# Kernel tuning notes

Measured on AMD Instinct MI355X. Metric: run time of the kernel, lower is better.

The kernel has to match this reference:

```python
import jax, jax.numpy as jnp
import numpy as np

B, S, DIN, DOUT = 4, 2048, 4096, 4096
W_SCALE = 64.0   # makes round(weight*scale) produce non-trivial int8 values
X_SCALE = 16.0   # input_scale so x*scale truncates to non-zero int32 values


def setup_inputs() -> dict:
    key = jax.random.key(0)
    k1, k2, k3 = jax.random.split(key, 3)
    # kaiming_uniform fan_in: bound = sqrt(6/fan_in)
    bound = float(np.sqrt(6.0 / DIN))
    weight = jax.random.uniform(k1, (DOUT, DIN), jnp.float32, -bound, bound)
    x = jax.random.normal(k2, (B, S, DIN), jnp.float32)
    bias = jax.random.normal(k3, (DOUT,), jnp.float32) * 0.01
    weight_scale = jnp.full((DOUT,), W_SCALE, jnp.float32)
    input_scale = jnp.full((1,), X_SCALE, jnp.float32)
    return {"x": x, "weight": weight, "bias": bias,
            "weight_scale": weight_scale, "input_scale": input_scale}


def reference(x, weight, bias, weight_scale, input_scale):
    # x = x * input_scale (pre-scale path of forward)
    xs = x * input_scale
    # fake-quant weights: round to int8 with wraparound, like torch .to(int8)
    w_int = jnp.round(weight * weight_scale[:, None]).astype(jnp.int8)
    # x.to(torch.int32): truncation toward zero
    x_int = xs.astype(jnp.int32)
    # F.linear on the integer-valued tensors (computed in f32: values are exact ints)
    acc = jnp.einsum('bsd,od->bso', x_int.astype(jnp.float32),
                     w_int.astype(jnp.float32))
    acc = acc + bias  # bias added inside linear
    # dequant: divide by per-channel weight_scale and the scalar input_scale
    out = acc / (weight_scale * input_scale)
    return out
```

## Files before the change

### kernel.cpp

```cpp
#include <hip/hip_runtime.h>

#define GM 8192
#define GN 4096
#define GK 4096

#define BM 256
#define BN 256
#define BK 64
#define NTILE (GK / BK)
#define SLOT 32768

using int4v = __attribute__((ext_vector_type(4))) int;

__global__ __launch_bounds__(256) void quant_xw_k(
    const float4* __restrict__ x, unsigned int* __restrict__ xq,
    const float4* __restrict__ w, unsigned int* __restrict__ wq,
    const float* __restrict__ wscale, const float* __restrict__ iscale,
    int n4x, int n4tot) {
    const float xs = *iscale;
    const int stride = gridDim.x * blockDim.x;
    for (int i = blockIdx.x * blockDim.x + threadIdx.x; i < n4tot; i += stride) {
        if (i < n4x) {
            float4 v = x[i];
            int q0 = (int)(v.x * xs);
            int q1 = (int)(v.y * xs);
            int q2 = (int)(v.z * xs);
            int q3 = (int)(v.w * xs);
            xq[i] = (unsigned int)(q0 & 0xff)
                  | ((unsigned int)(q1 & 0xff) << 8)
                  | ((unsigned int)(q2 & 0xff) << 16)
                  | ((unsigned int)(q3 & 0xff) << 24);
        } else {
            int j = i - n4x;
            float s = wscale[j >> 10];
            float4 v = w[j];
            int q0 = (int)rintf(v.x * s);
            int q1 = (int)rintf(v.y * s);
            int q2 = (int)rintf(v.z * s);
            int q3 = (int)rintf(v.w * s);
            wq[j] = (unsigned int)(q0 & 0xff)
                  | ((unsigned int)(q1 & 0xff) << 8)
                  | ((unsigned int)(q2 & 0xff) << 16)
                  | ((unsigned int)(q3 & 0xff) << 24);
        }
    }
}

__global__ __launch_bounds__(512, 2) void qlinear_gemm_i8(
    const signed char* __restrict__ Aq,
    const signed char* __restrict__ Bq,
    const float* __restrict__ bias,
    const float* __restrict__ wscale,
    const float* __restrict__ iscale,
    float* __restrict__ C) {
    __shared__ signed char smem[2 * SLOT];

    const int tid  = threadIdx.x;
    const int wave = tid >> 6;
    const int lane = tid & 63;
    const int m0 = blockIdx.x * BM;
    const int n0 = blockIdx.y * BN;
    const int wm = (wave >> 2) * 128;
    const int wn = (wave & 3) * 64;

    int4v acc[8][4];
#pragma unroll
    for (int i = 0; i < 8; ++i)
#pragma unroll
        for (int j = 0; j < 4; ++j)
            acc[i][j] = int4v{0, 0, 0, 0};

    const int kc = ((tid & 3) ^ ((tid >> 3) & 3)) * 16;
    const signed char* gA  = Aq + (size_t)(m0 + (tid >> 2)) * GK + kc;
    const signed char* gA2 = gA + (size_t)128 * GK;
    const signed char* gB  = Bq + (size_t)(n0 + (tid >> 2)) * GK + kc;
    const signed char* gB2 = gB + (size_t)128 * GK;
    const int dst = tid * 16;

    const int pos = (((lane >> 4) ^ ((lane >> 1) & 3))) * 16;
    const int fAo = (wm + (lane & 15)) * 64 + pos;
    const int fBo = 16384 + (wn + (lane & 15)) * 64 + pos;

#define GLL16(g, l)                                                     \
    __builtin_amdgcn_global_load_lds(                                   \
        (__attribute__((address_space(1))) void*)(void*)(g),            \
        (__attribute__((address_space(3))) void*)(void*)(l), 16, 0, 0)

#define STAGE(kb, soff)                                                 \
    do {                                                                \
        GLL16(gA  + (kb), smem + (soff) + dst);                         \
        GLL16(gA2 + (kb), smem + (soff) + 8192 + dst);                  \
        GLL16(gB  + (kb), smem + (soff) + 16384 + dst);                 \
        GLL16(gB2 + (kb), smem + (soff) + 24576 + dst);                 \
    } while (0)

#define DSR(off) (*(const int4v*)(smem + (off)))
#define MFMA(A, B, Cc) __builtin_amdgcn_mfma_i32_16x16x64_i8(A, B, Cc, 0, 0, 0)

#define PH(q)                                                           \
    __builtin_amdgcn_s_barrier();                                       \
    asm volatile("s_waitcnt lgkmcnt(0)" ::: "memory");                  \
    __builtin_amdgcn_sched_barrier(0);                                  \
    __builtin_amdgcn_s_setprio(1);                                      \
    acc[2*(q)  ][0] = MFMA(pa0, bfr0, acc[2*(q)  ][0]);                 \
    acc[2*(q)+1][0] = MFMA(pa1, bfr0, acc[2*(q)+1][0]);                 \
    acc[2*(q)  ][1] = MFMA(pa0, bfr1, acc[2*(q)  ][1]);                 \
    acc[2*(q)+1][1] = MFMA(pa1, bfr1, acc[2*(q)+1][1]);                 \
    acc[2*(q)  ][2] = MFMA(pa0, bfr2, acc[2*(q)  ][2]);                 \
    acc[2*(q)+1][2] = MFMA(pa1, bfr2, acc[2*(q)+1][2]);                 \
    acc[2*(q)  ][3] = MFMA(pa0, bfr3, acc[2*(q)  ][3]);                 \
    acc[2*(q)+1][3] = MFMA(pa1, bfr3, acc[2*(q)+1][3]);                 \
    __builtin_amdgcn_s_setprio(0);                                      \
    __builtin_amdgcn_s_barrier();

#define HALF(SOFF, STAGE_CODE)                                          \
    do {                                                                \
        STAGE_CODE;                                                     \
        bfr0 = DSR((SOFF) + fBo);                                       \
        bfr1 = DSR((SOFF) + fBo + 1024);                                \
        bfr2 = DSR((SOFF) + fBo + 2048);                                \
        bfr3 = DSR((SOFF) + fBo + 3072);                                \
        pa0  = DSR((SOFF) + fAo);                                       \
        pa1  = DSR((SOFF) + fAo + 1024);                                \
        PH(0)                                                           \
        pa0 = DSR((SOFF) + fAo + 2048);                                 \
        pa1 = DSR((SOFF) + fAo + 3072);                                 \
        PH(1)                                                           \
        pa0 = DSR((SOFF) + fAo + 4096);                                 \
        pa1 = DSR((SOFF) + fAo + 5120);                                 \
        PH(2)                                                           \
        pa0 = DSR((SOFF) + fAo + 6144);                                 \
        pa1 = DSR((SOFF) + fAo + 7168);                                 \
        asm volatile("s_waitcnt vmcnt(0)" ::: "memory");                \
        PH(3)                                                           \
    } while (0)

    STAGE(0, 0);
    asm volatile("s_waitcnt vmcnt(0)" ::: "memory");
    __builtin_amdgcn_s_barrier();
    __builtin_amdgcn_sched_barrier(0);

    int4v bfr0, bfr1, bfr2, bfr3, pa0, pa1;
    int kA = BK;
    int kB = 2 * BK;
    for (int it = 0; it < NTILE / 2; ++it) {
        HALF(0,    { STAGE(kA, SLOT); kA += 2 * BK; });
        HALF(SLOT, { if (kB < GK) { STAGE(kB, 0); kB += 2 * BK; } });
    }

    const float isc = *iscale;
#pragma unroll
    for (int ni = 0; ni < 4; ++ni) {
        const int col = n0 + wn + ni * 16 + (lane & 15);
        const float bs_ = bias[col];
        const float inv = 1.0f / (wscale[col] * isc);
#pragma unroll
        for (int mi = 0; mi < 8; ++mi) {
            const int row0 = m0 + wm + mi * 16 + (lane >> 4) * 4;
#pragma unroll
            for (int r = 0; r < 4; ++r) {
                C[(size_t)(row0 + r) * GN + col] =
                    ((float)acc[mi][ni][r] + bs_) * inv;
            }
        }
    }
#undef HALF
#undef PH
#undef DSR
#undef MFMA
#undef STAGE
#undef GLL16
}

extern "C" void kernel_launch(void* const* d_in, const int* in_sizes, int n_in,
                              void* d_out, int out_size, void* d_ws, size_t ws_size,
                              hipStream_t stream) {
    const float* x      = (const float*)d_in[0];
    const float* w      = (const float*)d_in[1];
    const float* bias   = (const float*)d_in[2];
    const float* wscale = (const float*)d_in[3];
    const float* iscale = (const float*)d_in[4];
    float* out = (float*)d_out;

    signed char* xq = (signed char*)d_ws;
    signed char* wq = xq + (size_t)GM * GK;

    const int n4x = GM * GK / 4;
    const int n4w = GN * GK / 4;
    quant_xw_k<<<3072, 256, 0, stream>>>((const float4*)x, (unsigned int*)xq,
                                         (const float4*)w, (unsigned int*)wq,
                                         wscale, iscale, n4x, n4x + n4w);

    dim3 grid(GM / BM, GN / BN);
    qlinear_gemm_i8<<<grid, 512, 0, stream>>>(xq, wq, bias, wscale, iscale, out);
}
```

Before: 411.7 us.

## Load B fragments directly to registers and triple-buffer A tiles in LDS

The weight (B) operand is no longer staged through shared memory. Each wave loads its B fragments straight from global memory into registers, double-buffered across iterations. The A tiles move to a three-slot LDS ring with a deeper prefetch distance, and each iteration has a single barrier instead of eight. This removes LDS traffic and barriers for B at the cost of uncoalesced-ish global reads for B (each wave reads its own rows, duplicated across the two M-waves) and higher register pressure.

```diff
diff --git a/kernel.cpp b/kernel.cpp
--- a/kernel.cpp
+++ b/kernel.cpp
@@ -8,7 +8,7 @@
 #define BN 256
 #define BK 64
 #define NTILE (GK / BK)
-#define SLOT 32768
+#define ASLOT 16384
 
 using int4v = __attribute__((ext_vector_type(4))) int;
 
@@ -53,7 +53,7 @@
     const float* __restrict__ wscale,
     const float* __restrict__ iscale,
     float* __restrict__ C) {
-    __shared__ signed char smem[2 * SLOT];
+    __shared__ signed char smem[3 * ASLOT];
 
     const int tid  = threadIdx.x;
     const int wave = tid >> 6;
@@ -73,79 +73,115 @@
     const int kc = ((tid & 3) ^ ((tid >> 3) & 3)) * 16;
     const signed char* gA  = Aq + (size_t)(m0 + (tid >> 2)) * GK + kc;
     const signed char* gA2 = gA + (size_t)128 * GK;
-    const signed char* gB  = Bq + (size_t)(n0 + (tid >> 2)) * GK + kc;
-    const signed char* gB2 = gB + (size_t)128 * GK;
     const int dst = tid * 16;
 
     const int pos = (((lane >> 4) ^ ((lane >> 1) & 3))) * 16;
     const int fAo = (wm + (lane & 15)) * 64 + pos;
-    const int fBo = 16384 + (wn + (lane & 15)) * 64 + pos;
+
+    const signed char* gB0 =
+        Bq + (size_t)(n0 + wn + (lane & 15)) * GK + ((lane >> 4) * 16);
+    const signed char* gB1 = gB0 + (size_t)16 * GK;
+    const signed char* gB2 = gB0 + (size_t)32 * GK;
+    const signed char* gB3 = gB0 + (size_t)48 * GK;
 
 #define GLL16(g, l)                                                     \
     __builtin_amdgcn_global_load_lds(                                   \
         (__attribute__((address_space(1))) void*)(void*)(g),            \
         (__attribute__((address_space(3))) void*)(void*)(l), 16, 0, 0)
 
-#define STAGE(kb, soff)                                                 \
+#define STAGE_A(kb, soff)                                               \
     do {                                                                \
         GLL16(gA  + (kb), smem + (soff) + dst);                         \
         GLL16(gA2 + (kb), smem + (soff) + 8192 + dst);                  \
-        GLL16(gB  + (kb), smem + (soff) + 16384 + dst);                 \
-        GLL16(gB2 + (kb), smem + (soff) + 24576 + dst);                 \
     } while (0)
 
-#define DSR(off) (*(const int4v*)(smem + (off)))
-#define MFMA(A, B, Cc) __builtin_amdgcn_mfma_i32_16x16x64_i8(A, B, Cc, 0, 0, 0)
-
-#define PH(q)                                                           \
-    __builtin_amdgcn_s_barrier();                                       \
-    asm volatile("s_waitcnt lgkmcnt(0)" ::: "memory");                  \
-    __builtin_amdgcn_sched_barrier(0);                                  \
-    __builtin_amdgcn_s_setprio(1);                                      \
-    acc[2*(q)  ][0] = MFMA(pa0, bfr0, acc[2*(q)  ][0]);                 \
-    acc[2*(q)+1][0] = MFMA(pa1, bfr0, acc[2*(q)+1][0]);                 \
-    acc[2*(q)  ][1] = MFMA(pa0, bfr1, acc[2*(q)  ][1]);                 \
-    acc[2*(q)+1][1] = MFMA(pa1, bfr1, acc[2*(q)+1][1]);                 \
-    acc[2*(q)  ][2] = MFMA(pa0, bfr2, acc[2*(q)  ][2]);                 \
-    acc[2*(q)+1][2] = MFMA(pa1, bfr2, acc[2*(q)+1][2]);                 \
-    acc[2*(q)  ][3] = MFMA(pa0, bfr3, acc[2*(q)  ][3]);                 \
-    acc[2*(q)+1][3] = MFMA(pa1, bfr3, acc[2*(q)+1][3]);                 \
-    __builtin_amdgcn_s_setprio(0);                                      \
+#define SB __builtin_amdgcn_sched_barrier(0)
+#define MFMA_I8(A, B, Cc) __builtin_amdgcn_mfma_i32_16x16x64_i8(A, B, Cc, 0, 0, 0)
+
+#define SUBITER(Bc0, Bc1, Bc2, Bc3, Bn0, Bn1, Bn2, Bn3)                 \
+    do {                                                                \
+        Bn0 = *(const int4v*)(gB0 + kbB);                               \
+        Bn1 = *(const int4v*)(gB1 + kbB);                               \
+        Bn2 = *(const int4v*)(gB2 + kbB);                               \
+        Bn3 = *(const int4v*)(gB3 + kbB);                               \
+        kbB += BK; if (kbB >= GK) kbB = 0;                              \
+        SB;                                                             \
+        STAGE_A(kst, sC);                                               \
+        kst += BK; if (kst >= GK) kst = 0;                              \
+        SB;                                                             \
+        {                                                               \
+            const signed char* fA = smem + sA + fAo;                    \
+            int4v a0 = *(const int4v*)(fA);                             \
+            int4v a1 = *(const int4v*)(fA + 1024);                      \
+            int4v a2 = *(const int4v*)(fA + 2048);                      \
+            int4v a3 = *(const int4v*)(fA + 3072);                      \
+            int4v a4 = *(const int4v*)(fA + 4096);                      \
+            int4v a5 = *(const int4v*)(fA + 5120);                      \
+            int4v a6 = *(const int4v*)(fA + 6144);                      \
+            int4v a7 = *(const int4v*)(fA + 7168);                      \
+            asm volatile("s_waitcnt vmcnt(8) lgkmcnt(0)" ::: "memory"); \
+            SB;                                                         \
+            __builtin_amdgcn_s_setprio(1);                              \
+            acc[0][0] = MFMA_I8(a0, Bc0, acc[0][0]);                    \
+            acc[1][0] = MFMA_I8(a1, Bc0, acc[1][0]);                    \
+            acc[2][0] = MFMA_I8(a2, Bc0, acc[2][0]);                    \
+            acc[3][0] = MFMA_I8(a3, Bc0, acc[3][0]);                    \
+            acc[4][0] = MFMA_I8(a4, Bc0, acc[4][0]);                    \
+            acc[5][0] = MFMA_I8(a5, Bc0, acc[5][0]);                    \
+            acc[6][0] = MFMA_I8(a6, Bc0, acc[6][0]);                    \
+            acc[7][0] = MFMA_I8(a7, Bc0, acc[7][0]);                    \
+            acc[0][1] = MFMA_I8(a0, Bc1, acc[0][1]);                    \
+            acc[1][1] = MFMA_I8(a1, Bc1, acc[1][1]);                    \
+            acc[2][1] = MFMA_I8(a2, Bc1, acc[2][1]);                    \
+            acc[3][1] = MFMA_I8(a3, Bc1, acc[3][1]);                    \
+            acc[4][1] = MFMA_I8(a4, Bc1, acc[4][1]);                    \
+            acc[5][1] = MFMA_I8(a5, Bc1, acc[5][1]);                    \
+            acc[6][1] = MFMA_I8(a6, Bc1, acc[6][1]);                    \
+            acc[7][1] = MFMA_I8(a7, Bc1, acc[7][1]);                    \
+            acc[0][2] = MFMA_I8(a0, Bc2, acc[0][2]);                    \
+            acc[1][2] = MFMA_I8(a1, Bc2, acc[1][2]);                    \
+            acc[2][2] = MFMA_I8(a2, Bc2, acc[2][2]);                    \
+            acc[3][2] = MFMA_I8(a3, Bc2, acc[3][2]);                    \
+            acc[4][2] = MFMA_I8(a4, Bc2, acc[4][2]);                    \
+            acc[5][2] = MFMA_I8(a5, Bc2, acc[5][2]);                    \
+            acc[6][2] = MFMA_I8(a6, Bc2, acc[6][2]);                    \
+            acc[7][2] = MFMA_I8(a7, Bc2, acc[7][2]);                    \
+            acc[0][3] = MFMA_I8(a0, Bc3, acc[0][3]);                    \
+            acc[1][3] = MFMA_I8(a1, Bc3, acc[1][3]);                    \
+            acc[2][3] = MFMA_I8(a2, Bc3, acc[2][3]);                    \
+            acc[3][3] = MFMA_I8(a3, Bc3, acc[3][3]);                    \
+            acc[4][3] = MFMA_I8(a4, Bc3, acc[4][3]);                    \
+            acc[5][3] = MFMA_I8(a5, Bc3, acc[5][3]);                    \
+            acc[6][3] = MFMA_I8(a6, Bc3, acc[6][3]);                    \
+            acc[7][3] = MFMA_I8(a7, Bc3, acc[7][3]);                    \
+            __builtin_amdgcn_s_setprio(0);                              \
+        }                                                               \
+        asm volatile("s_waitcnt vmcnt(6)" ::: "memory");                \
+        __builtin_amdgcn_s_barrier();                                   \
+        SB;                                                             \
+        { int t_ = sA; sA = sB_; sB_ = sC; sC = t_; }                   \
+    } while (0)
+
+    STAGE_A(0, 0);
+    SB;
+    int4v bX0 = *(const int4v*)(gB0);
+    int4v bX1 = *(const int4v*)(gB1);
+    int4v bX2 = *(const int4v*)(gB2);
+    int4v bX3 = *(const int4v*)(gB3);
+    SB;
+    STAGE_A(BK, ASLOT);
+    SB;
+    asm volatile("s_waitcnt vmcnt(6)" ::: "memory");
     __builtin_amdgcn_s_barrier();
-
-#define HALF(SOFF, STAGE_CODE)                                          \
-    do {                                                                \
-        STAGE_CODE;                                                     \
-        bfr0 = DSR((SOFF) + fBo);                                       \
-        bfr1 = DSR((SOFF) + fBo + 1024);                                \
-        bfr2 = DSR((SOFF) + fBo + 2048);                                \
-        bfr3 = DSR((SOFF) + fBo + 3072);                                \
-        pa0  = DSR((SOFF) + fAo);                                       \
-        pa1  = DSR((SOFF) + fAo + 1024);                                \
-        PH(0)                                                           \
-        pa0 = DSR((SOFF) + fAo + 2048);                                 \
-        pa1 = DSR((SOFF) + fAo + 3072);                                 \
-        PH(1)                                                           \
-        pa0 = DSR((SOFF) + fAo + 4096);                                 \
-        pa1 = DSR((SOFF) + fAo + 5120);                                 \
-        PH(2)                                                           \
-        pa0 = DSR((SOFF) + fAo + 6144);                                 \
-        pa1 = DSR((SOFF) + fAo + 7168);                                 \
-        asm volatile("s_waitcnt vmcnt(0)" ::: "memory");                \
-        PH(3)                                                           \
-    } while (0)
-
-    STAGE(0, 0);
-    asm volatile("s_waitcnt vmcnt(0)" ::: "memory");
-    __builtin_amdgcn_s_barrier();
-    __builtin_amdgcn_sched_barrier(0);
-
-    int4v bfr0, bfr1, bfr2, bfr3, pa0, pa1;
-    int kA = BK;
-    int kB = 2 * BK;
+    SB;
+
+    int4v bY0, bY1, bY2, bY3;
+    int sA = 0, sB_ = ASLOT, sC = 2 * ASLOT;
+    int kbB = BK;
+    int kst = 2 * BK;
     for (int it = 0; it < NTILE / 2; ++it) {
-        HALF(0,    { STAGE(kA, SLOT); kA += 2 * BK; });
-        HALF(SLOT, { if (kB < GK) { STAGE(kB, 0); kB += 2 * BK; } });
+        SUBITER(bX0, bX1, bX2, bX3, bY0, bY1, bY2, bY3);
+        SUBITER(bY0, bY1, bY2, bY3, bX0, bX1, bX2, bX3);
     }
 
     const float isc = *iscale;
@@ -164,11 +200,10 @@
             }
         }
     }
-#undef HALF
-#undef PH
-#undef DSR
-#undef MFMA
-#undef STAGE
+#undef SUBITER
+#undef MFMA_I8
+#undef SB
+#undef STAGE_A
 #undef GLL16
 }
 
```

Result: slower. 458.5 us (+11.4%).
